# Optimization experiments

Measured on AMD Instinct MI355X. Metric: run time of the kernel, lower is better.

## Reference

```python
import jax, jax.numpy as jnp
import numpy as np

EMBED_DIM = 768
NUM_HEADS = 12
HEAD_DIM = EMBED_DIM // NUM_HEADS
MAX_REL = 50
B, L = 4, 1024


def setup_inputs() -> dict:
    key = jax.random.key(0)
    ks = jax.random.split(key, 8)
    query = jax.random.normal(ks[0], (B, L, EMBED_DIM), dtype=jnp.float32)
    k_in = jax.random.normal(ks[1], (B, L, EMBED_DIM), dtype=jnp.float32)
    v_in = jax.random.normal(ks[2], (B, L, EMBED_DIM), dtype=jnp.float32)
    # monotone float timestamps per batch (arange fill)
    patch_indices = jnp.arange(B * L, dtype=jnp.float32).reshape(B, L)
    std = 1.0 / np.sqrt(EMBED_DIM)
    in_proj_w = jax.random.normal(ks[3], (3 * EMBED_DIM, EMBED_DIM), dtype=jnp.float32) * std
    in_proj_b = jnp.zeros((3 * EMBED_DIM,), dtype=jnp.float32)
    out_proj_w = jax.random.normal(ks[4], (EMBED_DIM, EMBED_DIM), dtype=jnp.float32) * std
    out_proj_b = jnp.zeros((EMBED_DIM,), dtype=jnp.float32)
    rel_bias = jax.random.truncated_normal(ks[5], -2.0, 2.0, (NUM_HEADS, 2 * MAX_REL + 1), dtype=jnp.float32) * 0.1
    return {"query": query, "key": k_in, "value": v_in, "patch_indices": patch_indices,
            "in_proj_w": in_proj_w, "in_proj_b": in_proj_b,
            "out_proj_w": out_proj_w, "out_proj_b": out_proj_b, "rel_bias": rel_bias}


def _attention(query, patch_indices, in_proj_w, in_proj_b, out_proj_w, out_proj_b, rel_bias):
    Bq, Lq, D = query.shape
    H, hd, M = NUM_HEADS, HEAD_DIM, MAX_REL
    qkv = query @ in_proj_w.T + in_proj_b            # [B,L,3D]
    q, k, v = jnp.split(qkv, 3, axis=-1)
    q = q.reshape(Bq, Lq, H, hd).transpose(0, 2, 1, 3) * (hd ** -0.5)
    k = k.reshape(Bq, Lq, H, hd).transpose(0, 2, 1, 3)
    v = v.reshape(Bq, Lq, H, hd).transpose(0, 2, 1, 3)
    scores = jnp.einsum('bhld,bhmd->bhlm', q, k)     # [B,H,L,L]
    # sequence-position relative bias
    idxs = jnp.arange(Lq)
    rel_pos = jnp.clip(idxs[None, :] - idxs[:, None], -M, M) + M   # [L,L]
    scores = scores + rel_bias[:, rel_pos][None]                   # [1,H,L,L]
    # data-dependent relative-time bias
    deltas = patch_indices[:, 1:] - patch_indices[:, :-1]          # [B,L-1]
    dt = jnp.nanmedian(deltas, axis=1)
    dt = jnp.where(jnp.isfinite(dt) & (dt > 0), dt, 1.0)[:, None, None]
    rel_time = patch_indices[:, :, None] - patch_indices[:, None, :]  # [B,L,L]
    invalid = jnp.isnan(rel_time) | (rel_time < -M) | (rel_time > M)
    rel_time = jnp.where(invalid, 0.0, rel_time)
    rel_idx = (jnp.clip(jnp.round(rel_time / dt), -M, M) + M).astype(jnp.int32)  # [B,L,L]
    bias = jnp.take(rel_bias, rel_idx, axis=1)       # [H,B,L,L]
    scores = scores + jnp.moveaxis(bias, 0, 1)       # [B,H,L,L]
    probs = jax.nn.softmax(scores, axis=-1)
    out = jnp.einsum('bhlm,bhmd->bhld', probs, v)
    out = out.transpose(0, 2, 1, 3).reshape(Bq, Lq, D)
    return out @ out_proj_w.T + out_proj_b


def reference(query, key, value, patch_indices, in_proj_w, in_proj_b, out_proj_w, out_proj_b, rel_bias):
    # NOTE: the original module ignores key/value and builds qkv from query.
    return _attention(query, patch_indices, in_proj_w, in_proj_b, out_proj_w, out_proj_b, rel_bias)
```

## Files before the change

kernel.cpp:

```cpp
#include <hip/hip_runtime.h>
#include <hip/hip_bf16.h>

#define BB 4
#define LL 1024
#define DD 768
#define HH 12
#define HD 64
#define MREL 50
#define NBIAS 101
#define GK 768
#define STR 72
#define BXS 68

#define NEG_INF (-__builtin_inff())

#define QB_F   ((size_t)0)
#define KB_F   ((size_t)1572864)
#define VTB_F  ((size_t)3145728)
#define XBF_F  ((size_t)4718592)
#define WIBF_F ((size_t)6291456)
#define WOBF_F ((size_t)7176192)
#define BIDX_F ((size_t)7471104)
#define DT_F   ((size_t)9568256)

#define NQ4  (BB*LL*DD)
#define NWI4 (3*DD*DD)

typedef __attribute__((ext_vector_type(8)))  short bf16x8;
typedef __attribute__((ext_vector_type(4)))  float f32x4;
typedef __attribute__((ext_vector_type(16))) float f32x16;
typedef __attribute__((ext_vector_type(4)))  unsigned int u32x4;

__device__ __forceinline__ unsigned short f2bf(float f) {
    unsigned u = __float_as_uint(f);
    u += 0x7fffu + ((u >> 16) & 1u);
    return (unsigned short)(u >> 16);
}

__device__ __forceinline__ void gload_lds16(const void* g, void* l) {
    __builtin_amdgcn_global_load_lds(
        (const __attribute__((address_space(1))) void*)g,
        (__attribute__((address_space(3))) void*)l, 16, 0, 0);
}

__global__ __launch_bounds__(256) void prep_kernel(
    const float* __restrict__ patch, float* __restrict__ dt,
    const float* __restrict__ q, const float* __restrict__ wi, const float* __restrict__ wo,
    unsigned short* __restrict__ qd_, unsigned short* __restrict__ wid,
    unsigned short* __restrict__ wod) {
    int tid = threadIdx.x;
    if (blockIdx.x >= 4) {
        int i = ((blockIdx.x - 4) * 256 + tid) * 4;
        const float* src; unsigned short* dst; int off;
        if (i < NQ4)              { src = q;  dst = qd_; off = i; }
        else if (i < NQ4 + NWI4)  { src = wi; dst = wid; off = i - NQ4; }
        else                      { src = wo; dst = wod; off = i - NQ4 - NWI4; }
        float4 v = *(const float4*)&src[off];
        ushort4 o;
        o.x = f2bf(v.x); o.y = f2bf(v.y); o.z = f2bf(v.z); o.w = f2bf(v.w);
        *(ushort4*)&dst[off] = o;
        return;
    }
    __shared__ __align__(16) float del[1024];
    __shared__ __align__(16) unsigned long long key64[1024];
    __shared__ int nvalid;
    __shared__ float acc;
    int b = blockIdx.x;
    if (tid == 0) { nvalid = 0; acc = 0.f; }
    __syncthreads();
    int cnt = 0;
#pragma unroll
    for (int r = 0; r < 4; ++r) {
        int i = tid + r * 256;
        float v = __builtin_nanf("");
        if (i < LL - 1) {
            v = patch[b * LL + i + 1] - patch[b * LL + i];
            if (v == v) ++cnt;
        }
        del[i] = v;
        unsigned bits = (v == v) ? __float_as_uint(v) : 0x7FC00000u;
        unsigned ordk = (bits & 0x80000000u) ? ~bits : (bits | 0x80000000u);
        key64[i] = ((unsigned long long)ordk << 10) | (unsigned)i;
    }
    atomicAdd(&nvalid, cnt);
    __syncthreads();
    int i0 = tid, i1 = tid + 256, i2 = tid + 512, i3 = tid + 768;
    float v0 = del[i0], v1 = del[i1], v2 = del[i2], v3 = del[i3];
    unsigned long long k0 = key64[i0], k1 = key64[i1], k2 = key64[i2], k3 = key64[i3];
    int c0 = 0, c1 = 0, c2 = 0, c3 = 0;
#define CMPK(kx) { unsigned long long _k = (kx); \
    c0 += (_k < k0) ? 1 : 0; c1 += (_k < k1) ? 1 : 0; \
    c2 += (_k < k2) ? 1 : 0; c3 += (_k < k3) ? 1 : 0; }
    for (int j = 0; j < 1024; j += 8) {
        ulonglong2 a = *(const ulonglong2*)&key64[j];
        ulonglong2 bq = *(const ulonglong2*)&key64[j + 2];
        ulonglong2 cq = *(const ulonglong2*)&key64[j + 4];
        ulonglong2 dq = *(const ulonglong2*)&key64[j + 6];
        CMPK(a.x); CMPK(a.y); CMPK(bq.x); CMPK(bq.y);
        CMPK(cq.x); CMPK(cq.y); CMPK(dq.x); CMPK(dq.y);
    }
#undef CMPK
    int n = nvalid;
#define FIN(vr, cr) if (vr == vr) { \
    if (n & 1) { if (cr == n / 2) atomicAdd(&acc, vr); } \
    else { if (cr == n / 2 - 1 || cr == n / 2) atomicAdd(&acc, 0.5f * vr); } }
    FIN(v0, c0); FIN(v1, c1); FIN(v2, c2); FIN(v3, c3);
#undef FIN
    __syncthreads();
    if (tid == 0) {
        float m = acc;
        float res = (n > 0 && m == m && fabsf(m) != __builtin_inff() && m > 0.f) ? m : 1.0f;
        dt[b] = res;
    }
}

__global__ __launch_bounds__(256) void bidx_kernel(const float* __restrict__ patch,
                                                   const float* __restrict__ dtb,
                                                   unsigned short* __restrict__ bidx) {
    int flat = (blockIdx.x * 256 + threadIdx.x) * 8;
    int b = flat >> 20;
    int rem = flat & 1048575;
    int i = rem >> 10;
    int j0 = rem & 1023;
    float pi = patch[b * LL + i];
    float inv_dt = 1.0f / dtb[b];
    float4 pa = *(const float4*)&patch[b * LL + j0];
    float4 pb4 = *(const float4*)&patch[b * LL + j0 + 4];
    unsigned out[4];
#define MK(pj, jofs, dst, shift) { \
    int d = (j0 + jofs) - i; d = d < -MREL ? -MREL : (d > MREL ? MREL : d); \
    float rt = pi - (pj); \
    if (!(rt == rt) || rt < -(float)MREL || rt > (float)MREL) rt = 0.f; \
    float fr = fminf(fmaxf(rintf(rt * inv_dt), -(float)MREL), (float)MREL); \
    unsigned u = (unsigned)(d + MREL) | (((unsigned)((int)fr + MREL)) << 8); \
    dst |= (u << shift); }
    unsigned t;
    t = 0; MK(pa.x, 0, t, 0); MK(pa.y, 1, t, 16); out[0] = t;
    t = 0; MK(pa.z, 2, t, 0); MK(pa.w, 3, t, 16); out[1] = t;
    t = 0; MK(pb4.x, 4, t, 0); MK(pb4.y, 5, t, 16); out[2] = t;
    t = 0; MK(pb4.z, 6, t, 0); MK(pb4.w, 7, t, 16); out[3] = t;
#undef MK
    *(uint4*)&bidx[flat] = *(uint4*)&out[0];
}

#define GEMM_CORE(TN_, RB_, NT_)                                               \
    __shared__ __align__(16) unsigned short smem_g[64 * 64 + TN_ * 64];        \
    unsigned short* As = smem_g;                                               \
    unsigned short* Bs = smem_g + 64 * 64;                                     \
    int tid = threadIdx.x;                                                     \
    int m0 = blockIdx.x << 6, n0 = blockIdx.y * TN_;                           \
    int lane = tid & 63, w = tid >> 6;                                         \
    int wn = w * (TN_ / 4);                                                    \
    int srow = tid >> 3, scol = (tid & 7) << 3;                                \
    const unsigned short* Ag = Ab + (size_t)(m0 + srow) * GK + scol;           \
    const unsigned short* Bg = Wb + (size_t)(n0 + srow) * GK + scol;           \
    f32x4 acc[4][NT_];                                                         \
    _Pragma("unroll") for (int i = 0; i < 4; ++i)                              \
        _Pragma("unroll") for (int j = 0; j < NT_; ++j)                        \
            acc[i][j] = (f32x4){0.f, 0.f, 0.f, 0.f};                           \
    int qd_ = lane >> 4;                                                       \
    int rA = lane & 15, rB = wn + (lane & 15);                                 \
    for (int kc = 0; kc < GK; kc += 64) {                                      \
        __syncthreads();                                                       \
        _Pragma("unroll") for (int r = 0; r < 2; ++r)                          \
            gload_lds16(Ag + (size_t)(r * 32) * GK + kc, As + tid * 8 + r * 2048); \
        _Pragma("unroll") for (int r = 0; r < RB_; ++r)                        \
            gload_lds16(Bg + (size_t)(r * 32) * GK + kc, Bs + tid * 8 + r * 2048); \
        __syncthreads();                                                       \
        _Pragma("unroll") for (int ks = 0; ks < 2; ++ks) {                     \
            bf16x8 af[4], bfr[NT_];                                            \
            _Pragma("unroll") for (int t = 0; t < 4; ++t)                      \
                af[t] = *(const bf16x8*)&As[(rA + t * 16) * 64 + ks * 32 + qd_ * 8]; \
            _Pragma("unroll") for (int t = 0; t < NT_; ++t)                    \
                bfr[t] = *(const bf16x8*)&Bs[(rB + t * 16) * 64 + ks * 32 + qd_ * 8]; \
            _Pragma("unroll") for (int i = 0; i < 4; ++i)                      \
                _Pragma("unroll") for (int j = 0; j < NT_; ++j)                \
                    acc[i][j] = __builtin_amdgcn_mfma_f32_16x16x32_bf16(       \
                        af[i], bfr[j], acc[i][j], 0, 0, 0);                    \
        }                                                                      \
    }                                                                          \
    int colL = lane & 15, rq = lane >> 4;

__global__ __launch_bounds__(256) void qkv_gemm(
    const unsigned short* __restrict__ Ab, const unsigned short* __restrict__ Wb,
    const float* __restrict__ bias,
    unsigned short* __restrict__ qb, unsigned short* __restrict__ kb,
    unsigned short* __restrict__ vtb) {
    GEMM_CORE(128, 4, 2);
    int sec = n0 / DD;
    if (sec == 2) {
        __syncthreads();
        unsigned short* Ts = smem_g;
#pragma unroll
        for (int j = 0; j < 2; ++j) {
            int nl = wn + j * 16 + colL;
            float bn = bias[n0 + nl];
#pragma unroll
            for (int i = 0; i < 4; ++i) {
                ushort4 o;
                o.x = f2bf(acc[i][j][0] + bn);
                o.y = f2bf(acc[i][j][1] + bn);
                o.z = f2bf(acc[i][j][2] + bn);
                o.w = f2bf(acc[i][j][3] + bn);
                *(ushort4*)&Ts[nl * 72 + i * 16 + rq * 4] = o;
            }
        }
        __syncthreads();
        int row = tid >> 1, half = tid & 1;
        int d768 = n0 + row - 2 * DD;
        int hh = d768 >> 6, dd = d768 & 63;
        unsigned short* dst = vtb + (((size_t)(m0 >> 10) * HH + hh) * HD + dd) * LL
                              + (m0 & 1023) + half * 32;
#pragma unroll
        for (int k = 0; k < 4; ++k)
            *(uint4*)&dst[k * 8] = *(const uint4*)&Ts[row * 72 + half * 32 + k * 8];
        return;
    }
    float scale = (sec == 0) ? 0.18033688011112042f : 1.0f;
#pragma unroll
    for (int j = 0; j < 2; ++j) {
        int n = n0 + wn + j * 16 + colL;
        int d768 = n - sec * DD;
        int hh = d768 >> 6, dd = d768 & 63;
        float bn = bias[n];
#pragma unroll
        for (int i = 0; i < 4; ++i) {
            int rowb = m0 + i * 16 + rq * 4;
#pragma unroll
            for (int r = 0; r < 4; ++r) {
                int m = rowb + r;
                int bidx = m >> 10, l = m & 1023;
                unsigned short val = f2bf((acc[i][j][r] + bn) * scale);
                if (sec == 0)
                    qb[(((size_t)bidx * HH + hh) * LL + l) * HD + dd] = val;
                else
                    kb[(((size_t)bidx * HH + hh) * LL + l) * HD + dd] = val;
            }
        }
    }
}

__global__ __launch_bounds__(256) void out_gemm(
    const unsigned short* __restrict__ Ab, const unsigned short* __restrict__ Wb,
    const float* __restrict__ bias, float* __restrict__ C) {
    GEMM_CORE(64, 2, 1);
    {
        int n = n0 + wn + colL;
        float bn = bias[n];
#pragma unroll
        for (int i = 0; i < 4; ++i) {
            int rowb = m0 + i * 16 + rq * 4;
#pragma unroll
            for (int r = 0; r < 4; ++r)
                C[(size_t)(rowb + r) * DD + n] = acc[i][0][r] + bn;
        }
    }
}

__global__ __launch_bounds__(256) void attn_kernel(
    const unsigned short* __restrict__ QB, const unsigned short* __restrict__ KB,
    const unsigned short* __restrict__ VTB, const unsigned short* __restrict__ BIDX,
    const float* __restrict__ relb, unsigned short* __restrict__ aout) {
    __shared__ __align__(16) unsigned short smem[2 * 64 * STR + 64 * BXS];
    __shared__ float sb[NBIAS];
    __shared__ float psum_s[128];
    __shared__ float linv_s[64];
    unsigned short* Ks  = smem;
    unsigned short* Vt  = smem + 64 * STR;
    unsigned short* Bxs = smem + 2 * 64 * STR;
    float* fcomb = (float*)smem;

    int tid = threadIdx.x;
    int w = tid >> 6, lane = tid & 63, li = lane & 31, qd = lane >> 5;
    int jt = w & 1, it = w >> 1;
    int bh = blockIdx.x, b = bh / HH, h = bh - b * HH;
    int q0 = blockIdx.y << 6;
    if (tid < NBIAS) sb[tid] = relb[h * NBIAS + tid] * 1.44269504088896340736f;
    int i_loc = it * 32 + li;
    int i_abs = q0 + i_loc;
    bf16x8 kq[4];
    const unsigned short* qrow = QB + ((size_t)bh * LL + i_abs) * HD + qd * 8;
#pragma unroll
    for (int ks = 0; ks < 4; ++ks) kq[ks] = *(const bf16x8*)(qrow + ks * 16);
    float l_run = 0.f;
    f32x16 O0, O1;
#pragma unroll
    for (int r = 0; r < 16; ++r) { O0[r] = 0.f; O1[r] = 0.f; }
    int srow = tid >> 3, sc = (tid & 7) << 3;
    const unsigned short* kgb = KB + (size_t)bh * LL * HD;
    const unsigned short* vgb = VTB + (size_t)bh * HD * LL;
    const unsigned short* bxg = BIDX + ((size_t)b << 20) + (size_t)q0 * 1024;
    bf16x8 kvr[2], vvr[2], bxr[2];
#pragma unroll
    for (int rep = 0; rep < 2; ++rep) {
        int r = srow + rep * 32;
        kvr[rep] = *(const bf16x8*)(kgb + (size_t)r * HD + sc);
        vvr[rep] = *(const bf16x8*)(vgb + (size_t)r * LL + sc);
        bxr[rep] = *(const bf16x8*)(bxg + (size_t)r * 1024 + sc);
    }
    __syncthreads();
    float sb0 = sb[0], sb100 = sb[100];
    for (int kt = 0; kt < 16; ++kt) {
        __syncthreads();
#pragma unroll
        for (int rep = 0; rep < 2; ++rep) {
            int r = srow + rep * 32;
            *(bf16x8*)&Ks[r * STR + sc] = kvr[rep];
            *(bf16x8*)&Vt[r * STR + sc] = vvr[rep];
            *(bf16x8*)&Bxs[r * BXS + sc] = bxr[rep];
        }
        if (kt + 1 < 16) {
#pragma unroll
            for (int rep = 0; rep < 2; ++rep) {
                int r = srow + rep * 32;
                kvr[rep] = *(const bf16x8*)(kgb + (size_t)((kt + 1) * 64 + r) * HD + sc);
                vvr[rep] = *(const bf16x8*)(vgb + (size_t)r * LL + (kt + 1) * 64 + sc);
                bxr[rep] = *(const bf16x8*)(bxg + (size_t)r * 1024 + (kt + 1) * 64 + sc);
            }
        }
        __syncthreads();
        f32x16 st;
#pragma unroll
        for (int r = 0; r < 16; ++r) st[r] = 0.f;
        __builtin_amdgcn_s_setprio(1);
#pragma unroll
        for (int ks = 0; ks < 4; ++ks) {
            bf16x8 ak = *(const bf16x8*)&Ks[(jt * 32 + li) * STR + ks * 16 + qd * 8];
            st = __builtin_amdgcn_mfma_f32_32x32x16_bf16(ak, kq[ks], st, 0, 0, 0);
        }
        __builtin_amdgcn_s_setprio(0);
        int delta = (kt << 6) + (jt << 5) - q0 - (it << 5);
        if (delta >= 81 || delta <= -81) {
            float db = (delta >= 81) ? sb100 : sb0;
#pragma unroll
            for (int g4 = 0; g4 < 4; ++g4) {
                ushort4 bi = *(const ushort4*)&Bxs[i_loc * BXS + jt * 32 + g4 * 8 + qd * 4];
#pragma unroll
                for (int q = 0; q < 4; ++q) {
                    int r = g4 * 4 + q;
                    unsigned u = (q == 0) ? bi.x : (q == 1) ? bi.y : (q == 2) ? bi.z : bi.w;
                    st[r] = st[r] + db + sb[u >> 8];
                }
            }
        } else {
#pragma unroll
            for (int g4 = 0; g4 < 4; ++g4) {
                ushort4 bi = *(const ushort4*)&Bxs[i_loc * BXS + jt * 32 + g4 * 8 + qd * 4];
#pragma unroll
                for (int q = 0; q < 4; ++q) {
                    int r = g4 * 4 + q;
                    unsigned u = (q == 0) ? bi.x : (q == 1) ? bi.y : (q == 2) ? bi.z : bi.w;
                    st[r] = st[r] + sb[u & 0xffu] + sb[u >> 8];
                }
            }
        }
        float rs = 0.f;
        unsigned W[8];
#pragma unroll
        for (int pr = 0; pr < 8; ++pr) {
            float p0 = __builtin_amdgcn_exp2f(st[2 * pr]);
            float p1 = __builtin_amdgcn_exp2f(st[2 * pr + 1]);
            rs += p0 + p1;
            unsigned wpk;
            asm("v_cvt_pk_bf16_f32 %0, %1, %2" : "=v"(wpk) : "v"(p0), "v"(p1));
            W[pr] = wpk;
        }
        rs += __shfl_xor(rs, 32);
        l_run += rs;
        auto s02 = __builtin_amdgcn_permlane32_swap(W[0], W[2], false, false);
        auto s13 = __builtin_amdgcn_permlane32_swap(W[1], W[3], false, false);
        auto s46 = __builtin_amdgcn_permlane32_swap(W[4], W[6], false, false);
        auto s57 = __builtin_amdgcn_permlane32_swap(W[5], W[7], false, false);
        u32x4 a0w = {(unsigned)s02[0], (unsigned)s13[0], (unsigned)s02[1], (unsigned)s13[1]};
        u32x4 a1w = {(unsigned)s46[0], (unsigned)s57[0], (unsigned)s46[1], (unsigned)s57[1]};
        bf16x8 ap0 = __builtin_bit_cast(bf16x8, a0w);
        bf16x8 ap1 = __builtin_bit_cast(bf16x8, a1w);
        {
            __builtin_amdgcn_s_setprio(1);
            bf16x8 bv;
            bv = *(const bf16x8*)&Vt[(li) * STR + jt * 32 + qd * 8];
            O0 = __builtin_amdgcn_mfma_f32_32x32x16_bf16(ap0, bv, O0, 0, 0, 0);
            bv = *(const bf16x8*)&Vt[(li) * STR + jt * 32 + 16 + qd * 8];
            O0 = __builtin_amdgcn_mfma_f32_32x32x16_bf16(ap1, bv, O0, 0, 0, 0);
            bv = *(const bf16x8*)&Vt[(32 + li) * STR + jt * 32 + qd * 8];
            O1 = __builtin_amdgcn_mfma_f32_32x32x16_bf16(ap0, bv, O1, 0, 0, 0);
            bv = *(const bf16x8*)&Vt[(32 + li) * STR + jt * 32 + 16 + qd * 8];
            O1 = __builtin_amdgcn_mfma_f32_32x32x16_bf16(ap1, bv, O1, 0, 0, 0);
            __builtin_amdgcn_s_setprio(0);
        }
    }
    if (qd == 0) psum_s[jt * 64 + i_loc] = l_run;
    __syncthreads();
    if (jt == 0 && qd == 0)
        linv_s[i_loc] = 1.0f / (psum_s[i_loc] + psum_s[64 + i_loc]);
    if (jt == 1) {
        int ibase = it * 32;
#pragma unroll
        for (int r = 0; r < 16; ++r) {
            int irow = (r & 3) + ((r >> 2) << 3) + (qd << 2);
            fcomb[(ibase + irow) * 64 + li] = O0[r];
            fcomb[(ibase + irow) * 64 + 32 + li] = O1[r];
        }
    }
    __syncthreads();
    if (jt == 0) {
        int ibase = it * 32;
#pragma unroll
        for (int r = 0; r < 16; ++r) {
            int irow = (r & 3) + ((r >> 2) << 3) + (qd << 2);
            float inv = linv_s[ibase + irow];
            float v0 = (O0[r] + fcomb[(ibase + irow) * 64 + li]) * inv;
            float v1 = (O1[r] + fcomb[(ibase + irow) * 64 + 32 + li]) * inv;
            size_t rowoff = (size_t)(b * LL + q0 + ibase + irow) * DD + h * HD;
            aout[rowoff + li] = f2bf(v0);
            aout[rowoff + 32 + li] = f2bf(v1);
        }
    }
}

extern "C" void kernel_launch(void* const* d_in, const int* in_sizes, int n_in,
                              void* d_out, int out_size, void* d_ws, size_t ws_size,
                              hipStream_t stream) {
    const float* query    = (const float*)d_in[0];
    const float* patch    = (const float*)d_in[3];
    const float* in_w     = (const float*)d_in[4];
    const float* in_b     = (const float*)d_in[5];
    const float* out_w    = (const float*)d_in[6];
    const float* out_b    = (const float*)d_in[7];
    const float* rel_bias = (const float*)d_in[8];
    float* ws  = (float*)d_ws;
    float* out = (float*)d_out;

    unsigned short* qb   = (unsigned short*)(ws + QB_F);
    unsigned short* kb   = (unsigned short*)(ws + KB_F);
    unsigned short* vtb  = (unsigned short*)(ws + VTB_F);
    unsigned short* xbf  = (unsigned short*)(ws + XBF_F);
    unsigned short* wibf = (unsigned short*)(ws + WIBF_F);
    unsigned short* wobf = (unsigned short*)(ws + WOBF_F);
    unsigned short* bidx = (unsigned short*)(ws + BIDX_F);

    prep_kernel<<<5380, 256, 0, stream>>>(patch, ws + DT_F, query, in_w, out_w,
                                          xbf, wibf, wobf);
    bidx_kernel<<<2048, 256, 0, stream>>>(patch, ws + DT_F, bidx);
    qkv_gemm<<<dim3(64, 18), 256, 0, stream>>>(xbf, wibf, in_b, qb, kb, vtb);
    attn_kernel<<<dim3(BB * HH, LL / 64), 256, 0, stream>>>(
        qb, kb, vtb, bidx, rel_bias, xbf);
    out_gemm<<<dim3(64, 12), 256, 0, stream>>>(xbf, wobf, out_b, out);
}
```

Before: 209.9 us.

## Use 128x128 GEMM tiles with LDS-staged coalesced Q/K epilogue; drop setprio

Both projection GEMMs move from 64-row tiles to 128x128 tiles with a 2x2 wave layout and a 4x4 accumulator grid per wave, which raises operand reuse per LDS load and reduces grid size. The Q/K epilogue now stages results through LDS and writes 16-byte vectors per row instead of scattered 2-byte stores. The s_setprio hints around the MFMA blocks in the attention kernel are removed. Fewer blocks (576 and 192) may underfill the GPU's compute units, and the larger accumulator set raises register pressure.

```diff
diff --git a/kernel.cpp b/kernel.cpp
--- a/kernel.cpp
+++ b/kernel.cpp
@@ -143,38 +143,38 @@
     *(uint4*)&bidx[flat] = *(uint4*)&out[0];
 }
 
-#define GEMM_CORE(TN_, RB_, NT_)                                               \
-    __shared__ __align__(16) unsigned short smem_g[64 * 64 + TN_ * 64];        \
+#define GEMM_MAIN(SMEMN)                                                       \
+    __shared__ __align__(16) unsigned short smem_g[SMEMN];                     \
     unsigned short* As = smem_g;                                               \
-    unsigned short* Bs = smem_g + 64 * 64;                                     \
+    unsigned short* Bs = smem_g + 8192;                                        \
     int tid = threadIdx.x;                                                     \
-    int m0 = blockIdx.x << 6, n0 = blockIdx.y * TN_;                           \
+    int m0 = blockIdx.x << 7, n0 = blockIdx.y << 7;                            \
     int lane = tid & 63, w = tid >> 6;                                         \
-    int wn = w * (TN_ / 4);                                                    \
+    int wr = w >> 1, wc = w & 1;                                               \
     int srow = tid >> 3, scol = (tid & 7) << 3;                                \
     const unsigned short* Ag = Ab + (size_t)(m0 + srow) * GK + scol;           \
     const unsigned short* Bg = Wb + (size_t)(n0 + srow) * GK + scol;           \
-    f32x4 acc[4][NT_];                                                         \
+    f32x4 acc[4][4];                                                           \
     _Pragma("unroll") for (int i = 0; i < 4; ++i)                              \
-        _Pragma("unroll") for (int j = 0; j < NT_; ++j)                        \
+        _Pragma("unroll") for (int j = 0; j < 4; ++j)                          \
             acc[i][j] = (f32x4){0.f, 0.f, 0.f, 0.f};                           \
-    int qd_ = lane >> 4;                                                       \
-    int rA = lane & 15, rB = wn + (lane & 15);                                 \
+    int qd_ = lane >> 4, rl = lane & 15;                                       \
+    int rA = wr * 64 + rl, rB = wc * 64 + rl;                                  \
     for (int kc = 0; kc < GK; kc += 64) {                                      \
         __syncthreads();                                                       \
-        _Pragma("unroll") for (int r = 0; r < 2; ++r)                          \
+        _Pragma("unroll") for (int r = 0; r < 4; ++r)                          \
             gload_lds16(Ag + (size_t)(r * 32) * GK + kc, As + tid * 8 + r * 2048); \
-        _Pragma("unroll") for (int r = 0; r < RB_; ++r)                        \
+        _Pragma("unroll") for (int r = 0; r < 4; ++r)                          \
             gload_lds16(Bg + (size_t)(r * 32) * GK + kc, Bs + tid * 8 + r * 2048); \
         __syncthreads();                                                       \
         _Pragma("unroll") for (int ks = 0; ks < 2; ++ks) {                     \
-            bf16x8 af[4], bfr[NT_];                                            \
+            bf16x8 af[4], bfr[4];                                              \
             _Pragma("unroll") for (int t = 0; t < 4; ++t)                      \
                 af[t] = *(const bf16x8*)&As[(rA + t * 16) * 64 + ks * 32 + qd_ * 8]; \
-            _Pragma("unroll") for (int t = 0; t < NT_; ++t)                    \
+            _Pragma("unroll") for (int t = 0; t < 4; ++t)                      \
                 bfr[t] = *(const bf16x8*)&Bs[(rB + t * 16) * 64 + ks * 32 + qd_ * 8]; \
             _Pragma("unroll") for (int i = 0; i < 4; ++i)                      \
-                _Pragma("unroll") for (int j = 0; j < NT_; ++j)                \
+                _Pragma("unroll") for (int j = 0; j < 4; ++j)                  \
                     acc[i][j] = __builtin_amdgcn_mfma_f32_16x16x32_bf16(       \
                         af[i], bfr[j], acc[i][j], 0, 0, 0);                    \
         }                                                                      \
@@ -186,15 +186,16 @@
     const float* __restrict__ bias,
     unsigned short* __restrict__ qb, unsigned short* __restrict__ kb,
     unsigned short* __restrict__ vtb) {
-    GEMM_CORE(128, 4, 2);
+    GEMM_MAIN(17408);
     int sec = n0 / DD;
+    int hh0 = (n0 - sec * DD) >> 6;
+    unsigned short* Ts = smem_g;
+    __syncthreads();
     if (sec == 2) {
-        __syncthreads();
-        unsigned short* Ts = smem_g;
-#pragma unroll
-        for (int j = 0; j < 2; ++j) {
-            int nl = wn + j * 16 + colL;
-            float bn = bias[n0 + nl];
+#pragma unroll
+        for (int j = 0; j < 4; ++j) {
+            int col_t = wc * 64 + j * 16 + colL;
+            float bn = bias[n0 + col_t];
 #pragma unroll
             for (int i = 0; i < 4; ++i) {
                 ushort4 o;
@@ -202,57 +203,57 @@
                 o.y = f2bf(acc[i][j][1] + bn);
                 o.z = f2bf(acc[i][j][2] + bn);
                 o.w = f2bf(acc[i][j][3] + bn);
-                *(ushort4*)&Ts[nl * 72 + i * 16 + rq * 4] = o;
+                *(ushort4*)&Ts[col_t * 136 + wr * 64 + i * 16 + rq * 4] = o;
             }
         }
         __syncthreads();
-        int row = tid >> 1, half = tid & 1;
-        int d768 = n0 + row - 2 * DD;
+        int nl = tid >> 1, half = tid & 1;
+        int d768 = n0 + nl - 2 * DD;
         int hh = d768 >> 6, dd = d768 & 63;
-        unsigned short* dst = vtb + (((size_t)(m0 >> 10) * HH + hh) * HD + dd) * LL
-                              + (m0 & 1023) + half * 32;
-#pragma unroll
-        for (int k = 0; k < 4; ++k)
-            *(uint4*)&dst[k * 8] = *(const uint4*)&Ts[row * 72 + half * 32 + k * 8];
-        return;
-    }
-    float scale = (sec == 0) ? 0.18033688011112042f : 1.0f;
-#pragma unroll
-    for (int j = 0; j < 2; ++j) {
-        int n = n0 + wn + j * 16 + colL;
-        int d768 = n - sec * DD;
-        int hh = d768 >> 6, dd = d768 & 63;
-        float bn = bias[n];
-#pragma unroll
-        for (int i = 0; i < 4; ++i) {
-            int rowb = m0 + i * 16 + rq * 4;
-#pragma unroll
-            for (int r = 0; r < 4; ++r) {
-                int m = rowb + r;
-                int bidx = m >> 10, l = m & 1023;
-                unsigned short val = f2bf((acc[i][j][r] + bn) * scale);
-                if (sec == 0)
-                    qb[(((size_t)bidx * HH + hh) * LL + l) * HD + dd] = val;
-                else
-                    kb[(((size_t)bidx * HH + hh) * LL + l) * HD + dd] = val;
+        int b = m0 >> 10, l0 = (m0 & 1023) + half * 64;
+        unsigned short* dst = vtb + (((size_t)b * HH + hh) * HD + dd) * LL + l0;
+#pragma unroll
+        for (int k = 0; k < 8; ++k)
+            *(uint4*)&dst[k * 8] = *(const uint4*)&Ts[nl * 136 + half * 64 + k * 8];
+    } else {
+        float scale = (sec == 0) ? 0.18033688011112042f : 1.0f;
+#pragma unroll
+        for (int j = 0; j < 4; ++j) {
+            int col_t = wc * 64 + j * 16 + colL;
+            float bn = bias[n0 + col_t];
+#pragma unroll
+            for (int i = 0; i < 4; ++i) {
+                int row_t = wr * 64 + i * 16 + rq * 4;
+#pragma unroll
+                for (int r = 0; r < 4; ++r)
+                    Ts[(row_t + r) * 136 + col_t] = f2bf((acc[i][j][r] + bn) * scale);
             }
         }
+        __syncthreads();
+        int ml = tid >> 1, half = tid & 1;
+        int b = (m0 + ml) >> 10, l = (m0 + ml) & 1023;
+        unsigned short* dst = (sec == 0 ? qb : kb)
+                              + (((size_t)b * HH + hh0 + half) * LL + l) * HD;
+#pragma unroll
+        for (int k = 0; k < 8; ++k)
+            *(uint4*)&dst[k * 8] = *(const uint4*)&Ts[ml * 136 + half * 64 + k * 8];
     }
 }
 
 __global__ __launch_bounds__(256) void out_gemm(
     const unsigned short* __restrict__ Ab, const unsigned short* __restrict__ Wb,
     const float* __restrict__ bias, float* __restrict__ C) {
-    GEMM_CORE(64, 2, 1);
-    {
-        int n = n0 + wn + colL;
+    GEMM_MAIN(16384);
+#pragma unroll
+    for (int j = 0; j < 4; ++j) {
+        int n = n0 + wc * 64 + j * 16 + colL;
         float bn = bias[n];
 #pragma unroll
         for (int i = 0; i < 4; ++i) {
-            int rowb = m0 + i * 16 + rq * 4;
+            int rowb = m0 + wr * 64 + i * 16 + rq * 4;
 #pragma unroll
             for (int r = 0; r < 4; ++r)
-                C[(size_t)(rowb + r) * DD + n] = acc[i][0][r] + bn;
+                C[(size_t)(rowb + r) * DD + n] = acc[i][j][r] + bn;
         }
     }
 }
@@ -322,13 +323,11 @@
         f32x16 st;
 #pragma unroll
         for (int r = 0; r < 16; ++r) st[r] = 0.f;
-        __builtin_amdgcn_s_setprio(1);
 #pragma unroll
         for (int ks = 0; ks < 4; ++ks) {
             bf16x8 ak = *(const bf16x8*)&Ks[(jt * 32 + li) * STR + ks * 16 + qd * 8];
             st = __builtin_amdgcn_mfma_f32_32x32x16_bf16(ak, kq[ks], st, 0, 0, 0);
         }
-        __builtin_amdgcn_s_setprio(0);
         int delta = (kt << 6) + (jt << 5) - q0 - (it << 5);
         if (delta >= 81 || delta <= -81) {
             float db = (delta >= 81) ? sb100 : sb0;
@@ -376,7 +375,6 @@
         bf16x8 ap0 = __builtin_bit_cast(bf16x8, a0w);
         bf16x8 ap1 = __builtin_bit_cast(bf16x8, a1w);
         {
-            __builtin_amdgcn_s_setprio(1);
             bf16x8 bv;
             bv = *(const bf16x8*)&Vt[(li) * STR + jt * 32 + qd * 8];
             O0 = __builtin_amdgcn_mfma_f32_32x32x16_bf16(ap0, bv, O0, 0, 0, 0);
@@ -386,7 +384,6 @@
             O1 = __builtin_amdgcn_mfma_f32_32x32x16_bf16(ap0, bv, O1, 0, 0, 0);
             bv = *(const bf16x8*)&Vt[(32 + li) * STR + jt * 32 + 16 + qd * 8];
             O1 = __builtin_amdgcn_mfma_f32_32x32x16_bf16(ap1, bv, O1, 0, 0, 0);
-            __builtin_amdgcn_s_setprio(0);
         }
     }
     if (qd == 0) psum_s[jt * 64 + i_loc] = l_run;
@@ -442,8 +439,8 @@
     prep_kernel<<<5380, 256, 0, stream>>>(patch, ws + DT_F, query, in_w, out_w,
                                           xbf, wibf, wobf);
     bidx_kernel<<<2048, 256, 0, stream>>>(patch, ws + DT_F, bidx);
-    qkv_gemm<<<dim3(64, 18), 256, 0, stream>>>(xbf, wibf, in_b, qb, kb, vtb);
+    qkv_gemm<<<dim3(32, 18), 256, 0, stream>>>(xbf, wibf, in_b, qb, kb, vtb);
     attn_kernel<<<dim3(BB * HH, LL / 64), 256, 0, stream>>>(
         qb, kb, vtb, bidx, rel_bias, xbf);
-    out_gemm<<<dim3(64, 12), 256, 0, stream>>>(xbf, wobf, out_b, out);
-}
+    out_gemm<<<dim3(32, 6), 256, 0, stream>>>(xbf, wobf, out_b, out);
+}
```

Result: slower. 217.1 us (+3.4%).
